# Kernel tuning notes

Measured on AMD Instinct MI355X. Metric: run time of the kernel, lower is better.

## Reference

```python
import jax, jax.numpy as jnp
import numpy as np

N_NODES = 50000
N_EDGES = 1600000
D_IN = 128
D_OUT = 32
ALPHA = 0.2  # LeakyReLU negative slope


def setup_inputs() -> dict:
    key = jax.random.key(0)
    k1, k2, k3, k4, k5, k6 = jax.random.split(key, 6)
    gain = float(np.sqrt(2.0))  # relu gain, xavier_normal-style scale
    X = jax.random.normal(k1, (N_NODES, D_IN), dtype=jnp.float32)
    weights = jax.random.normal(k2, (D_IN, D_OUT), dtype=jnp.float32) * (gain * np.sqrt(2.0 / (D_IN + D_OUT)))
    a0 = jax.random.normal(k3, (1, D_OUT), dtype=jnp.float32) * (gain * np.sqrt(2.0 / (1 + D_OUT)))
    a1 = jax.random.normal(k4, (1, D_OUT), dtype=jnp.float32) * (gain * np.sqrt(2.0 / (1 + D_OUT)))
    row_idx = jax.random.randint(k5, (N_EDGES,), 0, N_NODES, dtype=jnp.int32)
    col_idx = jax.random.randint(k6, (N_EDGES,), 0, N_NODES, dtype=jnp.int32)
    return {"X": X, "weights": weights, "a0": a0, "a1": a1,
            "row_idx": row_idx, "col_idx": col_idx}


def _minmax_norm(v):
    vmin = jnp.min(v)
    vmax = jnp.max(v)
    return (v - vmin) / (vmax - vmin)


def reference(X, weights, a0, a1, row_idx, col_idx):
    # X_prime = X @ W  -> [N, D]
    X_prime = X @ weights
    # Per-node partial scores; edge score e(i->j) = a0.X_prime[i] + a1.X_prime[j]
    s0 = jnp.sum(X_prime * a0, axis=-1)  # [N]
    s1 = jnp.sum(X_prime * a1, axis=-1)  # [N]
    att = s0[row_idx] + s1[col_idx]      # [E]
    # leakyrelu -> min-max normalize over all edges -> exp
    att = jax.nn.leaky_relu(att, negative_slope=ALPHA)
    att = jnp.exp(_minmax_norm(att))
    # rows_sum = SpMM(att, ones) = per-destination-row sum of edge weights
    rows_sum = jax.ops.segment_sum(att, row_idx, num_segments=N_NODES)  # [N]
    # h_prime = SpMM(att, X_prime) / rows_sum  (dropout p=0 -> identity)
    h = jax.ops.segment_sum(att[:, None] * X_prime[col_idx], row_idx,
                            num_segments=N_NODES)  # [N, D]
    return h / rows_sum[:, None]
```

## Files before the change

### kernel.cpp

```cpp
#include <hip/hip_runtime.h>
#include <math.h>

#define N_NODES 50000
#define N_EDGES 1600000
#define D_IN 128
#define D_OUT 32
#define ALPHA 0.2f

#define NB  512
#define RPB 98
#define HRPB 49
#define CAP 4096
#define CAPH 2048
#define PT  8
#define PB  512
#define EB  (PT * PB)
#define XNPB 32

__device__ __forceinline__ int enc_f(float x) {
    int i = __float_as_int(x);
    return i >= 0 ? i : (i ^ 0x7fffffff);
}
__device__ __forceinline__ float dec_f(int k) {
    return __int_as_float(k >= 0 ? k : (k ^ 0x7fffffff));
}

__global__ __launch_bounds__(256) void k_xw(const float* __restrict__ X,
                                            const float* __restrict__ W,
                                            const float* __restrict__ a0,
                                            const float* __restrict__ a1,
                                            float* __restrict__ Xp,
                                            float* __restrict__ s0,
                                            float* __restrict__ s1,
                                            int* __restrict__ minmax,
                                            int* __restrict__ gcount) {
    __shared__ float4 Wl4[D_IN * D_OUT / 4];
    __shared__ float4 Xl4[XNPB * D_IN / 4];
    const int tid = threadIdx.x;
    if (blockIdx.x == 0) {
        if (tid == 0) {
            minmax[0] = 0x7fffffff;
            minmax[1] = 0x80000000;
        }
        for (int i = tid; i < NB; i += 256) gcount[i] = 0;
    }
    const int node0 = blockIdx.x * XNPB;
    {
        const float4* W4 = (const float4*)W;
#pragma unroll
        for (int i = 0; i < 4; ++i) Wl4[tid + 256 * i] = W4[tid + 256 * i];
        const float4* X4 = (const float4*)X + (size_t)node0 * (D_IN / 4);
        const int lim = (min(XNPB, N_NODES - node0)) * (D_IN / 4);
#pragma unroll
        for (int i = 0; i < 4; ++i) {
            const int idx = tid + 256 * i;
            Xl4[idx] = (idx < lim) ? X4[idx] : make_float4(0.f, 0.f, 0.f, 0.f);
        }
    }
    __syncthreads();

    const int g = tid >> 3;
    const int l = tid & 7;
    const int node = node0 + g;
    const float4* xr = &Xl4[g * (D_IN / 4)];
    float ax = 0.f, ay = 0.f, az = 0.f, aw = 0.f;
#pragma unroll 4
    for (int kk = 0; kk < D_IN / 4; ++kk) {
        const float4 xv = xr[kk];
        const float4 w0 = Wl4[(4 * kk + 0) * 8 + l];
        const float4 w1 = Wl4[(4 * kk + 1) * 8 + l];
        const float4 w2 = Wl4[(4 * kk + 2) * 8 + l];
        const float4 w3 = Wl4[(4 * kk + 3) * 8 + l];
        ax += xv.x * w0.x + xv.y * w1.x + xv.z * w2.x + xv.w * w3.x;
        ay += xv.x * w0.y + xv.y * w1.y + xv.z * w2.y + xv.w * w3.y;
        az += xv.x * w0.z + xv.y * w1.z + xv.z * w2.z + xv.w * w3.z;
        aw += xv.x * w0.w + xv.y * w1.w + xv.z * w2.w + xv.w * w3.w;
    }
    if (node < N_NODES)
        ((float4*)Xp)[(size_t)node * 8 + l] = make_float4(ax, ay, az, aw);

    const float4 A0 = ((const float4*)a0)[l];
    const float4 A1 = ((const float4*)a1)[l];
    float v0 = ax * A0.x + ay * A0.y + az * A0.z + aw * A0.w;
    float v1 = ax * A1.x + ay * A1.y + az * A1.z + aw * A1.w;
#pragma unroll
    for (int m = 4; m >= 1; m >>= 1) {
        v0 += __shfl_xor(v0, m);
        v1 += __shfl_xor(v1, m);
    }
    if (l == 0 && node < N_NODES) { s0[node] = v0; s1[node] = v1; }
}

__global__ __launch_bounds__(PB) void k_part(const int* __restrict__ row,
                                             const int* __restrict__ col,
                                             const float* __restrict__ s0,
                                             const float* __restrict__ s1,
                                             int* __restrict__ gcount,
                                             int* __restrict__ minmax,
                                             uint2* __restrict__ gEdges) {
    __shared__ int hist[NB];
    __shared__ int lcur[NB];
    __shared__ int smn[PB / 64], smx[PB / 64];
    const int t = threadIdx.x;
    for (int i = t; i < NB; i += PB) hist[i] = 0;
    __syncthreads();

    const int base = blockIdx.x * EB;
    unsigned px[PT];
    float    fa[PT];
    int cnt = 0;
    int kmin = 0x7fffffff, kmax = 0x80000000;
#pragma unroll
    for (int i = 0; i < PT; ++i) {
        const int e = base + i * PB + t;
        if (e >= N_EDGES) break;
        const int r = row[e];
        const int c = col[e];
        float a = s0[r] + s1[c];
        a = a > 0.f ? a : ALPHA * a;
        const int k = enc_f(a);
        kmin = min(kmin, k);
        kmax = max(kmax, k);
        const unsigned b = (unsigned)r / RPB;
        const unsigned lr = (unsigned)r - b * RPB;
        px[cnt] = (b << 23) | (lr << 16) | (unsigned)c;
        fa[cnt] = a;
        ++cnt;
        atomicAdd(&hist[b], 1);
    }
    __syncthreads();
    for (int i = t; i < NB; i += PB) {
        const int h = hist[i];
        lcur[i] = h > 0 ? atomicAdd(&gcount[i], h) : 0;
    }
    __syncthreads();
    for (int j = 0; j < cnt; ++j) {
        const unsigned p = px[j];
        const unsigned b = p >> 23;
        const int pos = atomicAdd(&lcur[b], 1);
        gEdges[(size_t)b * CAP + pos] =
            make_uint2(p & 0x7FFFFFu, (unsigned)__float_as_int(fa[j]));
    }
#pragma unroll
    for (int m = 32; m >= 1; m >>= 1) {
        kmin = min(kmin, __shfl_xor(kmin, m));
        kmax = max(kmax, __shfl_xor(kmax, m));
    }
    const int wave = t >> 6;
    if ((t & 63) == 0) { smn[wave] = kmin; smx[wave] = kmax; }
    __syncthreads();
    if (t == 0) {
#pragma unroll
        for (int w = 1; w < PB / 64; ++w) {
            kmin = min(kmin, smn[w]);
            kmax = max(kmax, smx[w]);
        }
        atomicMin(&minmax[0], kmin);
        atomicMax(&minmax[1], kmax);
    }
}

__global__ __launch_bounds__(512, 8) void k_bucket(const int* __restrict__ gcount,
                                                   const uint2* __restrict__ gEdges,
                                                   const float* __restrict__ Xp,
                                                   const int* __restrict__ minmax,
                                                   float* __restrict__ out) {
    __shared__ unsigned short scol[CAPH];
    __shared__ float swt[CAPH];
    __shared__ int off[HRPB + 1];
    __shared__ int cur[HRPB];
    const int bid = blockIdx.x;
    const int b = bid >> 1;
    const int lo = (bid & 1) * HRPB;
    const int t = threadIdx.x;
    const float mn = dec_f(minmax[0]);
    const float mx = dec_f(minmax[1]);
    const float inv = 1.0f / (mx - mn);
    const int cnt = min(gcount[b], CAP);
    const uint2* eb = gEdges + (size_t)b * CAP;

    if (t < HRPB) cur[t] = 0;
    __syncthreads();
    for (int i = t; i < cnt; i += 512) {
        const int lrl = (int)(eb[i].x >> 16) - lo;
        if ((unsigned)lrl < (unsigned)HRPB) atomicAdd(&cur[lrl], 1);
    }
    __syncthreads();
    if (t == 0) {
        int run = 0;
#pragma unroll
        for (int r = 0; r < HRPB; ++r) { off[r] = run; run += cur[r]; }
        off[HRPB] = run;
    }
    __syncthreads();
    if (t < HRPB) cur[t] = off[t];
    __syncthreads();
    for (int i = t; i < cnt; i += 512) {
        const uint2 e = eb[i];
        const int lrl = (int)(e.x >> 16) - lo;
        if ((unsigned)lrl < (unsigned)HRPB) {
            const int p = atomicAdd(&cur[lrl], 1);
            scol[p] = (unsigned short)(e.x & 0xFFFFu);
            swt[p] = __expf((__int_as_float(e.y) - mn) * inv);
        }
    }
    __syncthreads();

    const int proc = t >> 5;
    const int d = t & 31;
    for (int lrl = proc; lrl < HRPB; lrl += 16) {
        const int s = off[lrl];
        const int e2 = off[lrl + 1];
        float ac0 = 0.f, ac1 = 0.f, ac2 = 0.f, ac3 = 0.f;
        float w0s = 0.f, w1s = 0.f, w2s = 0.f, w3s = 0.f;
        int i = s;
        for (; i + 3 < e2; i += 4) {
            const int c0 = scol[i];
            const int c1 = scol[i + 1];
            const int c2 = scol[i + 2];
            const int c3 = scol[i + 3];
            const float w0 = swt[i];
            const float w1 = swt[i + 1];
            const float w2 = swt[i + 2];
            const float w3 = swt[i + 3];
            ac0 += w0 * Xp[(size_t)c0 * D_OUT + d];
            ac1 += w1 * Xp[(size_t)c1 * D_OUT + d];
            ac2 += w2 * Xp[(size_t)c2 * D_OUT + d];
            ac3 += w3 * Xp[(size_t)c3 * D_OUT + d];
            w0s += w0; w1s += w1; w2s += w2; w3s += w3;
        }
        for (; i < e2; ++i) {
            const float w0 = swt[i];
            ac0 += w0 * Xp[(size_t)scol[i] * D_OUT + d];
            w0s += w0;
        }
        const int r = b * RPB + lo + lrl;
        if (r < N_NODES)
            out[(size_t)r * D_OUT + d] =
                (ac0 + ac1 + ac2 + ac3) / (w0s + w1s + w2s + w3s);
    }
}

extern "C" void kernel_launch(void* const* d_in, const int* in_sizes, int n_in,
                              void* d_out, int out_size, void* d_ws, size_t ws_size,
                              hipStream_t stream) {
    const float* X  = (const float*)d_in[0];
    const float* W  = (const float*)d_in[1];
    const float* a0 = (const float*)d_in[2];
    const float* a1 = (const float*)d_in[3];
    const int* row  = (const int*)d_in[4];
    const int* col  = (const int*)d_in[5];
    float* out = (float*)d_out;

    float* ws = (float*)d_ws;
    int*   minmax = (int*)ws;
    int*   gcount = (int*)(ws + 64);
    float* s0 = ws + 64 + 2048;
    float* s1 = s0 + 50048;
    float* Xp = s1 + 50048;
    uint2* gEdges = (uint2*)(Xp + (size_t)N_NODES * D_OUT);

    k_xw<<<(N_NODES + XNPB - 1) / XNPB, 256, 0, stream>>>(X, W, a0, a1, Xp, s0, s1,
                                                          minmax, gcount);
    k_part<<<(N_EDGES + EB - 1) / EB, PB, 0, stream>>>(row, col, s0, s1, gcount,
                                                       minmax, gEdges);
    k_bucket<<<NB * 2, 512, 0, stream>>>(gcount, gEdges, Xp, minmax, out);
}
```

Measured before the change: 155.9 us.

## Store Xp as bf16, shrink edge records, recompute scores in bucket kernel

The projected features Xp are now stored as bfloat16, which halves the bytes fetched by the gather in the aggregation kernel. Partitioned edge records drop the stored attention value and keep only a 32-bit packed index. The bucket kernel recomputes the LeakyReLU score from s0 (staged in shared memory) and s1. The partition kernel also reads row/col as int4 vectors when the block is full. This cuts global traffic at the cost of bf16 precision in the feature sum and extra s1 gathers.

```diff
diff --git a/kernel.cpp b/kernel.cpp
--- a/kernel.cpp
+++ b/kernel.cpp
@@ -1,4 +1,5 @@
 #include <hip/hip_runtime.h>
+#include <hip/hip_bf16.h>
 #include <math.h>
 
 #define N_NODES 50000
@@ -24,12 +25,19 @@
 __device__ __forceinline__ float dec_f(int k) {
     return __int_as_float(k >= 0 ? k : (k ^ 0x7fffffff));
 }
+__device__ __forceinline__ unsigned short f2bf(float x) {
+    __hip_bfloat16 h = __float2bfloat16(x);
+    return *(unsigned short*)&h;
+}
+__device__ __forceinline__ float bf2f(unsigned short u) {
+    return __uint_as_float((unsigned)u << 16);
+}
 
 __global__ __launch_bounds__(256) void k_xw(const float* __restrict__ X,
                                             const float* __restrict__ W,
                                             const float* __restrict__ a0,
                                             const float* __restrict__ a1,
-                                            float* __restrict__ Xp,
+                                            unsigned short* __restrict__ Xpb,
                                             float* __restrict__ s0,
                                             float* __restrict__ s1,
                                             int* __restrict__ minmax,
@@ -76,8 +84,12 @@
         az += xv.x * w0.z + xv.y * w1.z + xv.z * w2.z + xv.w * w3.z;
         aw += xv.x * w0.w + xv.y * w1.w + xv.z * w2.w + xv.w * w3.w;
     }
-    if (node < N_NODES)
-        ((float4*)Xp)[(size_t)node * 8 + l] = make_float4(ax, ay, az, aw);
+    if (node < N_NODES) {
+        uint2 pk;
+        pk.x = ((unsigned)f2bf(ay) << 16) | f2bf(ax);
+        pk.y = ((unsigned)f2bf(aw) << 16) | f2bf(az);
+        ((uint2*)Xpb)[(size_t)node * 8 + l] = pk;
+    }
 
     const float4 A0 = ((const float4*)a0)[l];
     const float4 A1 = ((const float4*)a1)[l];
@@ -97,7 +109,7 @@
                                              const float* __restrict__ s1,
                                              int* __restrict__ gcount,
                                              int* __restrict__ minmax,
-                                             uint2* __restrict__ gEdges) {
+                                             unsigned* __restrict__ gEdges) {
     __shared__ int hist[NB];
     __shared__ int lcur[NB];
     __shared__ int smn[PB / 64], smx[PB / 64];
@@ -107,26 +119,47 @@
 
     const int base = blockIdx.x * EB;
     unsigned px[PT];
-    float    fa[PT];
     int cnt = 0;
     int kmin = 0x7fffffff, kmax = 0x80000000;
-#pragma unroll
-    for (int i = 0; i < PT; ++i) {
-        const int e = base + i * PB + t;
-        if (e >= N_EDGES) break;
-        const int r = row[e];
-        const int c = col[e];
-        float a = s0[r] + s1[c];
-        a = a > 0.f ? a : ALPHA * a;
-        const int k = enc_f(a);
-        kmin = min(kmin, k);
-        kmax = max(kmax, k);
-        const unsigned b = (unsigned)r / RPB;
-        const unsigned lr = (unsigned)r - b * RPB;
-        px[cnt] = (b << 23) | (lr << 16) | (unsigned)c;
-        fa[cnt] = a;
-        ++cnt;
-        atomicAdd(&hist[b], 1);
+    if (base + EB <= N_EDGES) {
+#pragma unroll
+        for (int i = 0; i < PT / 4; ++i) {
+            const int4 r4 = ((const int4*)(row + base))[t + i * PB];
+            const int4 c4 = ((const int4*)(col + base))[t + i * PB];
+            const int rr[4] = {r4.x, r4.y, r4.z, r4.w};
+            const int cc[4] = {c4.x, c4.y, c4.z, c4.w};
+#pragma unroll
+            for (int j = 0; j < 4; ++j) {
+                const int r = rr[j];
+                const int c = cc[j];
+                float a = s0[r] + s1[c];
+                a = a > 0.f ? a : ALPHA * a;
+                const int k = enc_f(a);
+                kmin = min(kmin, k);
+                kmax = max(kmax, k);
+                const unsigned b = (unsigned)r / RPB;
+                const unsigned lr = (unsigned)r - b * RPB;
+                px[cnt++] = (b << 23) | (lr << 16) | (unsigned)c;
+                atomicAdd(&hist[b], 1);
+            }
+        }
+    } else {
+#pragma unroll
+        for (int i = 0; i < PT; ++i) {
+            const int e = base + i * PB + t;
+            if (e >= N_EDGES) break;
+            const int r = row[e];
+            const int c = col[e];
+            float a = s0[r] + s1[c];
+            a = a > 0.f ? a : ALPHA * a;
+            const int k = enc_f(a);
+            kmin = min(kmin, k);
+            kmax = max(kmax, k);
+            const unsigned b = (unsigned)r / RPB;
+            const unsigned lr = (unsigned)r - b * RPB;
+            px[cnt++] = (b << 23) | (lr << 16) | (unsigned)c;
+            atomicAdd(&hist[b], 1);
+        }
     }
     __syncthreads();
     for (int i = t; i < NB; i += PB) {
@@ -138,8 +171,7 @@
         const unsigned p = px[j];
         const unsigned b = p >> 23;
         const int pos = atomicAdd(&lcur[b], 1);
-        gEdges[(size_t)b * CAP + pos] =
-            make_uint2(p & 0x7FFFFFu, (unsigned)__float_as_int(fa[j]));
+        gEdges[(size_t)b * CAP + pos] = p & 0x7FFFFFu;
     }
 #pragma unroll
     for (int m = 32; m >= 1; m >>= 1) {
@@ -161,12 +193,15 @@
 }
 
 __global__ __launch_bounds__(512, 8) void k_bucket(const int* __restrict__ gcount,
-                                                   const uint2* __restrict__ gEdges,
-                                                   const float* __restrict__ Xp,
+                                                   const unsigned* __restrict__ gEdges,
+                                                   const unsigned short* __restrict__ Xpb,
+                                                   const float* __restrict__ s0,
+                                                   const float* __restrict__ s1,
                                                    const int* __restrict__ minmax,
                                                    float* __restrict__ out) {
     __shared__ unsigned short scol[CAPH];
     __shared__ float swt[CAPH];
+    __shared__ float s0l[HRPB];
     __shared__ int off[HRPB + 1];
     __shared__ int cur[HRPB];
     const int bid = blockIdx.x;
@@ -177,12 +212,16 @@
     const float mx = dec_f(minmax[1]);
     const float inv = 1.0f / (mx - mn);
     const int cnt = min(gcount[b], CAP);
-    const uint2* eb = gEdges + (size_t)b * CAP;
-
-    if (t < HRPB) cur[t] = 0;
+    const unsigned* eb = gEdges + (size_t)b * CAP;
+
+    if (t < HRPB) {
+        cur[t] = 0;
+        const int r = b * RPB + lo + t;
+        s0l[t] = (r < N_NODES) ? s0[r] : 0.f;
+    }
     __syncthreads();
     for (int i = t; i < cnt; i += 512) {
-        const int lrl = (int)(eb[i].x >> 16) - lo;
+        const int lrl = (int)(eb[i] >> 16) - lo;
         if ((unsigned)lrl < (unsigned)HRPB) atomicAdd(&cur[lrl], 1);
     }
     __syncthreads();
@@ -196,12 +235,15 @@
     if (t < HRPB) cur[t] = off[t];
     __syncthreads();
     for (int i = t; i < cnt; i += 512) {
-        const uint2 e = eb[i];
-        const int lrl = (int)(e.x >> 16) - lo;
+        const unsigned e = eb[i];
+        const int lrl = (int)(e >> 16) - lo;
         if ((unsigned)lrl < (unsigned)HRPB) {
+            const unsigned c = e & 0xFFFFu;
+            float a = s0l[lrl] + s1[c];
+            a = a > 0.f ? a : ALPHA * a;
             const int p = atomicAdd(&cur[lrl], 1);
-            scol[p] = (unsigned short)(e.x & 0xFFFFu);
-            swt[p] = __expf((__int_as_float(e.y) - mn) * inv);
+            scol[p] = (unsigned short)c;
+            swt[p] = __expf((a - mn) * inv);
         }
     }
     __syncthreads();
@@ -223,15 +265,15 @@
             const float w1 = swt[i + 1];
             const float w2 = swt[i + 2];
             const float w3 = swt[i + 3];
-            ac0 += w0 * Xp[(size_t)c0 * D_OUT + d];
-            ac1 += w1 * Xp[(size_t)c1 * D_OUT + d];
-            ac2 += w2 * Xp[(size_t)c2 * D_OUT + d];
-            ac3 += w3 * Xp[(size_t)c3 * D_OUT + d];
+            ac0 += w0 * bf2f(Xpb[(size_t)c0 * D_OUT + d]);
+            ac1 += w1 * bf2f(Xpb[(size_t)c1 * D_OUT + d]);
+            ac2 += w2 * bf2f(Xpb[(size_t)c2 * D_OUT + d]);
+            ac3 += w3 * bf2f(Xpb[(size_t)c3 * D_OUT + d]);
             w0s += w0; w1s += w1; w2s += w2; w3s += w3;
         }
         for (; i < e2; ++i) {
             const float w0 = swt[i];
-            ac0 += w0 * Xp[(size_t)scol[i] * D_OUT + d];
+            ac0 += w0 * bf2f(Xpb[(size_t)scol[i] * D_OUT + d]);
             w0s += w0;
         }
         const int r = b * RPB + lo + lrl;
@@ -257,12 +299,12 @@
     int*   gcount = (int*)(ws + 64);
     float* s0 = ws + 64 + 2048;
     float* s1 = s0 + 50048;
-    float* Xp = s1 + 50048;
-    uint2* gEdges = (uint2*)(Xp + (size_t)N_NODES * D_OUT);
-
-    k_xw<<<(N_NODES + XNPB - 1) / XNPB, 256, 0, stream>>>(X, W, a0, a1, Xp, s0, s1,
+    unsigned short* Xpb = (unsigned short*)(s1 + 50048);
+    unsigned* gEdges = (unsigned*)(s1 + 50048 + 800000);
+
+    k_xw<<<(N_NODES + XNPB - 1) / XNPB, 256, 0, stream>>>(X, W, a0, a1, Xpb, s0, s1,
                                                           minmax, gcount);
     k_part<<<(N_EDGES + EB - 1) / EB, PB, 0, stream>>>(row, col, s0, s1, gcount,
                                                        minmax, gEdges);
-    k_bucket<<<NB * 2, 512, 0, stream>>>(gcount, gEdges, Xp, minmax, out);
-}
+    k_bucket<<<NB * 2, 512, 0, stream>>>(gcount, gEdges, Xpb, s0, s1, minmax, out);
+}
```

Measured after the change: 157.7 us. Within noise of the previous version (+1.2%).
